# Kernel tuning notes

Hardware: AMD Instinct MI355X
Metric: run time of the kernel (lower is better)

Reference implementation:

```python
import jax, jax.numpy as jnp
import numpy as np
import math

B, T, O = 4, 1024, 128
D, H, L, V = 512, 8, 6, 128
M, EH = 100000, 4
EHD = D // EH
HD = D // H
TK = O + 2 * T
PAD_ID = 0
NGRAM = 4

def _primes():
    ps = []
    base = 131
    for h in range(EH):
        x = base + h * 1009
        row = []
        for _ in range(NGRAM):
            row.append(x % (2 ** 32))
            x = x * 31 + 1
        ps.append(row)
    return jnp.array(ps, dtype=jnp.uint32)

PRIMES = _primes()

def rmsnorm(x, scale, eps=1e-6):
    return x / jnp.sqrt(jnp.mean(jnp.square(x), axis=-1, keepdims=True) + eps) * scale

def precompute_freqs_cis(dim, max_len, theta=10000.0):
    freqs = 1.0 / theta ** (jnp.arange(0, dim, 2, dtype=jnp.float32) / dim)
    t = jnp.arange(max_len, dtype=jnp.float32)
    return jnp.exp(1j * jnp.outer(t, freqs))[None, :, None, :]  # (1, max_len, 1, dim/2)

def apply_rope(x, f):
    b, t, h, d = x.shape
    xc = jax.lax.complex(x[..., 0::2], x[..., 1::2])
    xr = xc * f
    return jnp.stack([xr.real, xr.imag], axis=-1).reshape(b, t, h, d)

def setup_inputs() -> dict:
    key = jax.random.key(0)
    ks = jax.random.split(key, 16)
    rn = lambda k, shp, s=0.02: jax.random.normal(k, shp, jnp.float32) * s
    logit = lambda p: float(np.log(p / (1.0 - p)))
    return {
        'tokens_w': jax.random.randint(ks[0], (B, T), 0, V, dtype=jnp.int32),
        'mem_ids': jax.random.randint(ks[1], (B, O), 0, V, dtype=jnp.int32),
        'mem_emb': jax.random.normal(ks[2], (B, O, D), jnp.float32),
        'ssum': jax.random.normal(ks[3], (B, D), jnp.float32),
        'embed_table': rn(ks[4], (V, D)),
        'engram_table': rn(ks[5], (M, EH, EHD)),
        'engram_gate': jnp.full((EH, EHD), -2.0, jnp.float32),
        'engram_scale': jnp.ones(D, jnp.float32),
        'mem_W': rn(ks[6], (D, D)), 'mem_b': jnp.zeros(D, jnp.float32),
        'mem_scale': jnp.ones(D, jnp.float32),
        'alpha_gate': jnp.full((D,), logit(0.1), jnp.float32),
        'ssum_W': rn(ks[7], (D, D)),
        'ln1': jnp.ones((L, D), jnp.float32),
        'qW': rn(ks[8], (L, D, D)), 'qb': jnp.zeros((L, D), jnp.float32),
        'kW': rn(ks[9], (L, D, D)), 'kb': jnp.zeros((L, D), jnp.float32),
        'vW': rn(ks[10], (L, D, D)), 'vb': jnp.zeros((L, D), jnp.float32),
        'oW': rn(ks[11], (L, D, D)), 'ob': jnp.zeros((L, D), jnp.float32),
        'ln2': jnp.ones((L, D), jnp.float32),
        'w_in': rn(ks[12], (L, D, 8 * D)),
        'w_out': rn(ks[13], (L, 4 * D, D)),
        'final_scale': jnp.ones(D, jnp.float32),
    }

def _forward(tokens_w, mem_ids, mem_emb, ssum, embed_table, engram_table, engram_gate,
             engram_scale, mem_W, mem_b, mem_scale, alpha_gate, ssum_W,
             ln1, qW, qb, kW, kb, vW, vb, oW, ob, ln2, w_in, w_out, final_scale):
    # token embedding
    x = embed_table[tokens_w]  # (B,T,D)
    # multi-head engram: rolling n-gram hash lookup
    cur = jnp.where(tokens_w == PAD_ID, 0, tokens_w).astype(jnp.uint32)
    prev = jnp.where(mem_ids == PAD_ID, 0, mem_ids).astype(jnp.uint32)
    full = jnp.concatenate([prev, cur], axis=1)  # (B, O+T)
    hs = jnp.zeros((B, T, EH), jnp.uint32)
    for i in range(NGRAM):
        chunk = full[:, O - i: O + T - i]
        hs = hs + chunk[:, :, None] * PRIMES[None, None, :, i]
    idx = (hs % jnp.uint32(M)).astype(jnp.int32)  # (B,T,EH)
    retr = engram_table[idx, jnp.arange(EH)[None, None, :], :]  # (B,T,EH,EHD)
    eng = (retr * jax.nn.sigmoid(engram_gate)[None, None]).reshape(B, T, D)
    eng = rmsnorm(eng, engram_scale)
    # memory adapter + state-sum injection
    mem_p = rmsnorm(mem_emb @ mem_W + mem_b, mem_scale)
    alpha = jax.nn.sigmoid(alpha_gate)
    x = x + (ssum @ ssum_W)[:, None, :] * alpha[None, None, :]
    kv_seq = jnp.concatenate([mem_p, eng, x], axis=1)  # (B, TK, D)
    # masks: mem fully visible, engram + current causal; pad invalid keys
    tril = jnp.tril(jnp.ones((T, T), bool))
    full_mask = jnp.concatenate([jnp.ones((T, O), bool), tril, tril], axis=1)
    valid_curr = tokens_w != PAD_ID
    valid_k = jnp.concatenate([jnp.ones((B, O), bool), valid_curr, valid_curr], axis=1)
    mask = full_mask[None, None] & valid_k[:, None, None, :]  # (B,1,T,TK)
    freqs = precompute_freqs_cis(HD, TK + 32)
    fq, fk = freqs[:, :T], freqs[:, :TK]
    scale = 1.0 / math.sqrt(HD)

    def block(cx, p):
        ln1_, qW_, qb_, kW_, kb_, vW_, vb_, oW_, ob_, ln2_, wi_, wo_ = p
        nx = rmsnorm(cx, ln1_)
        q = (nx @ qW_ + qb_).reshape(B, T, H, HD)
        k = (kv_seq @ kW_ + kb_).reshape(B, TK, H, HD)
        v = (kv_seq @ vW_ + vb_).reshape(B, TK, H, HD)
        q = apply_rope(q, fq)
        k = apply_rope(k, fk)
        scores = jnp.einsum('bqhd,bkhd->bhqk', q, k) * scale
        scores = jnp.where(mask, scores, -1e9)
        probs = jax.nn.softmax(scores, axis=-1)
        o = jnp.einsum('bhqk,bkhd->bqhd', probs, v).reshape(B, T, D)
        cx = cx + o @ oW_ + ob_
        n2 = rmsnorm(cx, ln2_)
        gate, val = jnp.split(n2 @ wi_, 2, axis=-1)
        cx = cx + (jax.nn.silu(gate) * val) @ wo_
        return cx, None

    curr_x, _ = jax.lax.scan(block, x, (ln1, qW, qb, kW, kb, vW, vb, oW, ob, ln2, w_in, w_out))
    return rmsnorm(curr_x, final_scale)

def reference(tokens_w, mem_ids, mem_emb, ssum, embed_table, engram_table, engram_gate,
              engram_scale, mem_W, mem_b, mem_scale, alpha_gate, ssum_W,
              ln1, qW, qb, kW, kb, vW, vb, oW, ob, ln2, w_in, w_out, final_scale):
    return _forward(tokens_w, mem_ids, mem_emb, ssum, embed_table, engram_table, engram_gate,
                    engram_scale, mem_W, mem_b, mem_scale, alpha_gate, ssum_W,
                    ln1, qW, qb, kW, kb, vW, vb, oW, ob, ln2, w_in, w_out, final_scale)
```

## Files before the change

### kernel.cpp

```cpp
#include <hip/hip_runtime.h>
#include <hip/hip_bf16.h>
#include <math.h>

#define B_ 4
#define T_ 1024
#define O_ 128
#define D_ 512
#define H_ 8
#define L_ 6
#define TK_ 2176
#define MM_ 100000
#define EH_ 4
#define EHD_ 128
#define HD_ 64

typedef float f32x4 __attribute__((ext_vector_type(4)));
typedef short bf16x8 __attribute__((ext_vector_type(8)));
typedef unsigned short u16;

__device__ __constant__ unsigned int PRIMES_[4][4] = {
  {131u,  4062u,  125923u, 3903614u},
  {1140u, 35341u, 1095572u, 33962733u},
  {2149u, 66620u, 2065221u, 64021852u},
  {3158u, 97899u, 3034870u, 94080971u},
};

__device__ __forceinline__ float wave_sum_f(float v) {
  #pragma unroll
  for (int off = 32; off; off >>= 1) v += __shfl_xor(v, off);
  return v;
}

__device__ __forceinline__ short f2bf(float f) {
  unsigned int u = __float_as_uint(f);
  unsigned int r = (u + 0x7fffu + ((u >> 16) & 1u)) >> 16;
  return (short)r;
}

__device__ __forceinline__ void gload16(const void* g, void* l) {
  __builtin_amdgcn_global_load_lds((const __attribute__((address_space(1))) void*)g,
                                   (__attribute__((address_space(3))) void*)l, 16, 0, 0);
}

__global__ __launch_bounds__(64) void rope_table_k(float* __restrict__ rc,
                                                   float* __restrict__ rs) {
  int i = blockIdx.x * 64 + threadIdx.x;
  int t = i >> 5, j = i & 31;
  float freq = __powf(10000.0f, -(float)j / 32.0f);
  float ang = (float)t * freq;
  rc[i] = cosf(ang);
  rs[i] = sinf(ang);
}

__global__ __launch_bounds__(256) void ssum_proj_k(const float* __restrict__ ssum,
                                                   const float* __restrict__ sW,
                                                   float* __restrict__ ssp) {
  int col = blockIdx.x * 256 + threadIdx.x;
  int b = blockIdx.y;
  float acc = 0.f;
  for (int d = 0; d < D_; ++d) acc += ssum[b * D_ + d] * sW[(size_t)d * D_ + col];
  ssp[b * D_ + col] = acc;
}

__global__ __launch_bounds__(256) void sgemm_k(const float* __restrict__ A,
                                               const float* __restrict__ W,
                                               const float* __restrict__ bias,
                                               float* __restrict__ C,
                                               int M, int N, int K) {
  __shared__ float As[16][68];
  __shared__ float Bs[16][68];
  int tid = threadIdx.x;
  int row0 = blockIdx.y * 64;
  int col0 = blockIdx.x * 64;
  int tx = tid & 15, ty = tid >> 4;
  int am = tid >> 2, ak = (tid & 3) * 4;
  int bk = tid >> 4, bc = (tid & 15) * 4;
  float acc[4][4] = {};
  for (int k0 = 0; k0 < K; k0 += 16) {
    float4 av = *reinterpret_cast<const float4*>(&A[(size_t)(row0 + am) * K + k0 + ak]);
    As[ak + 0][am] = av.x; As[ak + 1][am] = av.y; As[ak + 2][am] = av.z; As[ak + 3][am] = av.w;
    float4 bv = *reinterpret_cast<const float4*>(&W[(size_t)(k0 + bk) * N + col0 + bc]);
    *reinterpret_cast<float4*>(&Bs[bk][bc]) = bv;
    __syncthreads();
    #pragma unroll
    for (int kk = 0; kk < 16; ++kk) {
      float4 a4 = *reinterpret_cast<const float4*>(&As[kk][ty * 4]);
      float4 b4 = *reinterpret_cast<const float4*>(&Bs[kk][tx * 4]);
      float a[4] = {a4.x, a4.y, a4.z, a4.w};
      float b[4] = {b4.x, b4.y, b4.z, b4.w};
      #pragma unroll
      for (int i = 0; i < 4; ++i)
        #pragma unroll
        for (int j = 0; j < 4; ++j) acc[i][j] += a[i] * b[j];
    }
    __syncthreads();
  }
  int cbase = col0 + tx * 4;
  float4 b4 = *reinterpret_cast<const float4*>(&bias[cbase]);
  float bb[4] = {b4.x, b4.y, b4.z, b4.w};
  #pragma unroll
  for (int i = 0; i < 4; ++i) {
    int row = row0 + ty * 4 + i;
    *reinterpret_cast<float4*>(&C[(size_t)row * N + cbase]) =
        make_float4(acc[i][0] + bb[0], acc[i][1] + bb[1], acc[i][2] + bb[2], acc[i][3] + bb[3]);
  }
}

__device__ __forceinline__ void wconv_tile(const float* __restrict__ W, u16* __restrict__ wT,
                                           int K, int N) {
  __shared__ float s[64][65];
  int n0 = blockIdx.x * 64, k0 = blockIdx.y * 64;
  int tid = threadIdx.x;
  int kr = tid >> 4, nc = (tid & 15) * 4;
  #pragma unroll
  for (int kk = 0; kk < 4; ++kk) {
    float4 f = *reinterpret_cast<const float4*>(&W[(size_t)(k0 + kr + kk * 16) * N + n0 + nc]);
    s[kr + kk * 16][nc + 0] = f.x; s[kr + kk * 16][nc + 1] = f.y;
    s[kr + kk * 16][nc + 2] = f.z; s[kr + kk * 16][nc + 3] = f.w;
  }
  __syncthreads();
  int nr = tid >> 4, kc = (tid & 15) * 4;
  #pragma unroll
  for (int nn = 0; nn < 4; ++nn) {
    int n = nr + nn * 16;
    ushort4 o;
    o.x = (u16)f2bf(s[kc + 0][n]); o.y = (u16)f2bf(s[kc + 1][n]);
    o.z = (u16)f2bf(s[kc + 2][n]); o.w = (u16)f2bf(s[kc + 3][n]);
    *reinterpret_cast<ushort4*>(&wT[(size_t)(n0 + n) * K + k0 + kc]) = o;
  }
}

__global__ __launch_bounds__(256) void wconv_qkvo_k(const float* __restrict__ qW,
                                                    const float* __restrict__ kW,
                                                    const float* __restrict__ vW,
                                                    const float* __restrict__ oW,
                                                    u16* __restrict__ dst) {
  int z = blockIdx.z;
  int l = z >> 2, which = z & 3;
  const float* src = which == 0 ? qW : which == 1 ? kW : which == 2 ? vW : oW;
  wconv_tile(src + (size_t)l * D_ * D_, dst + (size_t)z * D_ * D_, D_, D_);
}

__global__ __launch_bounds__(256) void wconv_win_k(const float* __restrict__ w_in,
                                                   u16* __restrict__ dst) {
  int l = blockIdx.z;
  wconv_tile(w_in + (size_t)l * 512 * 4096, dst + (size_t)l * 4096 * 512, 512, 4096);
}

__global__ __launch_bounds__(256) void wconv_wout_k(const float* __restrict__ w_out,
                                                    u16* __restrict__ dst) {
  int l = blockIdx.z;
  wconv_tile(w_out + (size_t)l * 2048 * 512, dst + (size_t)l * 512 * 2048, 2048, 512);
}

template<int EPI>
__global__ __launch_bounds__(256) void gemm_sm_k(const u16* __restrict__ A,
                                                 const u16* __restrict__ Bt,
                                                 const float* __restrict__ bias,
                                                 void* __restrict__ Cout,
                                                 int M, int N, int K, int posmod,
                                                 const float* __restrict__ rc,
                                                 const float* __restrict__ rs) {
  __shared__ __align__(16) u16 As[2][64 * 32];
  __shared__ __align__(16) u16 Bs[2][64 * 32];
  int tid = threadIdx.x;
  int w = tid >> 6, lane = tid & 63;
  int lr = lane & 15, lg = lane >> 4;
  int row0 = blockIdx.y * 64, col0 = blockIdx.x * 64;
  int wr = w >> 1, wc = w & 1;
  f32x4 acc[2][2] = {};

  int srow = tid >> 2;
  int skel = (tid & 3) * 8;

  auto stage = [&](int buf, int k0) {
    gload16(A + (size_t)(row0 + srow) * K + k0 + skel, &As[buf][srow * 32 + skel]);
    gload16(Bt + (size_t)(col0 + srow) * K + k0 + skel, &Bs[buf][srow * 32 + skel]);
  };

  stage(0, 0);
  __syncthreads();
  int nk = K >> 5;
  int buf = 0;
  for (int t = 0; t < nk; ++t) {
    if (t + 1 < nk) stage(buf ^ 1, (t + 1) * 32);
    bf16x8 af[2], bf[2];
    #pragma unroll
    for (int i = 0; i < 2; ++i)
      af[i] = *reinterpret_cast<const bf16x8*>(&As[buf][(wr * 32 + i * 16 + lr) * 32 + lg * 8]);
    #pragma unroll
    for (int j = 0; j < 2; ++j)
      bf[j] = *reinterpret_cast<const bf16x8*>(&Bs[buf][(wc * 32 + j * 16 + lr) * 32 + lg * 8]);
    #pragma unroll
    for (int i = 0; i < 2; ++i)
      #pragma unroll
      for (int j = 0; j < 2; ++j)
        acc[i][j] = __builtin_amdgcn_mfma_f32_16x16x32_bf16(af[i], bf[j], acc[i][j], 0, 0, 0);
    __syncthreads();
    buf ^= 1;
  }

  #pragma unroll
  for (int j = 0; j < 2; ++j) {
    int col = col0 + wc * 32 + j * 16 + lr;
    float bs = bias ? bias[col] : 0.f;
    #pragma unroll
    for (int i = 0; i < 2; ++i) {
      #pragma unroll
      for (int r = 0; r < 4; ++r) {
        int row = row0 + wr * 32 + i * 16 + lg * 4 + r;
        float v = acc[i][j][r] + bs;
        if (EPI == 1) {
          int pos = row % posmod;
          int d = col & 63;
          float c = rc[(size_t)pos * 32 + (d >> 1)];
          float s = rs[(size_t)pos * 32 + (d >> 1)];
          float partner = __shfl_xor(v, 1);
          v = (d & 1) ? (partner * s + v * c) : (v * c - partner * s);
        }
        if (EPI == 2) {
          float* Cf = (float*)Cout;
          Cf[(size_t)row * N + col] += v;
        } else {
          u16* Cb = (u16*)Cout;
          Cb[(size_t)row * N + col] = (u16)f2bf(v);
        }
      }
    }
  }
}

__global__ __launch_bounds__(256) void kv_gemm_k(const u16* __restrict__ A,
                                                 const u16* __restrict__ wqkvoT,
                                                 const float* __restrict__ kbias_all,
                                                 const float* __restrict__ vbias_all,
                                                 u16* __restrict__ kb_base,
                                                 u16* __restrict__ vb_base,
                                                 const float* __restrict__ rc,
                                                 const float* __restrict__ rs,
                                                 int l0, size_t ostride) {
  __shared__ __align__(16) u16 As[2][128 * 32];
  __shared__ __align__(16) u16 Bk[2][64 * 32];
  __shared__ __align__(16) u16 Bv[2][64 * 32];
  const int K = 512, N = 512;
  int l = l0 + blockIdx.z;
  const u16* wkT = wqkvoT + ((size_t)l * 4 + 1) * (D_ * D_);
  const u16* wvT = wqkvoT + ((size_t)l * 4 + 2) * (D_ * D_);
  const float* kbias = kbias_all + l * D_;
  const float* vbias = vbias_all + l * D_;
  u16* kb = kb_base + (size_t)blockIdx.z * ostride;
  u16* vb = vb_base + (size_t)blockIdx.z * ostride;
  int tid = threadIdx.x;
  int w = tid >> 6, lane = tid & 63;
  int lr = lane & 15, lg = lane >> 4;
  int row0 = blockIdx.y * 128, col0 = blockIdx.x * 64;
  int wr = w >> 1, wc = w & 1;
  f32x4 ak_[4][2] = {};
  f32x4 av_[4][2] = {};

  int srow = lane >> 2;
  int skel = (lane & 3) * 8;

  auto stage = [&](int buf, int k0) {
    #pragma unroll
    for (int ci = 0; ci < 2; ++ci) {
      int c = w * 2 + ci;
      gload16(A + (size_t)(row0 + c * 16 + srow) * K + k0 + skel, &As[buf][c * 512]);
    }
    gload16(wkT + (size_t)(col0 + w * 16 + srow) * K + k0 + skel, &Bk[buf][w * 512]);
    gload16(wvT + (size_t)(col0 + w * 16 + srow) * K + k0 + skel, &Bv[buf][w * 512]);
  };

  stage(0, 0);
  __syncthreads();
  int buf = 0;
  for (int t = 0; t < 16; ++t) {
    if (t + 1 < 16) stage(buf ^ 1, (t + 1) * 32);
    bf16x8 af[4], bk[2], bv[2];
    #pragma unroll
    for (int i = 0; i < 4; ++i)
      af[i] = *reinterpret_cast<const bf16x8*>(&As[buf][(wr * 64 + i * 16 + lr) * 32 + lg * 8]);
    #pragma unroll
    for (int j = 0; j < 2; ++j) {
      bk[j] = *reinterpret_cast<const bf16x8*>(&Bk[buf][(wc * 32 + j * 16 + lr) * 32 + lg * 8]);
      bv[j] = *reinterpret_cast<const bf16x8*>(&Bv[buf][(wc * 32 + j * 16 + lr) * 32 + lg * 8]);
    }
    #pragma unroll
    for (int i = 0; i < 4; ++i)
      #pragma unroll
      for (int j = 0; j < 2; ++j) {
        ak_[i][j] = __builtin_amdgcn_mfma_f32_16x16x32_bf16(af[i], bk[j], ak_[i][j], 0, 0, 0);
        av_[i][j] = __builtin_amdgcn_mfma_f32_16x16x32_bf16(af[i], bv[j], av_[i][j], 0, 0, 0);
      }
    __syncthreads();
    buf ^= 1;
  }

  u16* stg = &As[0][0];
  __syncthreads();
  #pragma unroll
  for (int pass = 0; pass < 2; ++pass) {
    #pragma unroll
    for (int j = 0; j < 2; ++j) {
      int lcol = wc * 32 + j * 16 + lr;
      int gcol = col0 + lcol;
      float bs = pass ? vbias[gcol] : kbias[gcol];
      int d = gcol & 63;
      #pragma unroll
      for (int i = 0; i < 4; ++i) {
        #pragma unroll
        for (int r = 0; r < 4; ++r) {
          int lrow = wr * 64 + i * 16 + lg * 4 + r;
          float v = (pass ? av_[i][j][r] : ak_[i][j][r]) + bs;
          if (!pass) {
            int pos = (row0 + lrow) % TK_;
            float c = rc[(size_t)pos * 32 + (d >> 1)];
            float s = rs[(size_t)pos * 32 + (d >> 1)];
            float partner = __shfl_xor(v, 1);
            v = (d & 1) ? (partner * s + v * c) : (v * c - partner * s);
          }
          stg[lrow * 64 + lcol] = (u16)f2bf(v);
        }
      }
    }
    __syncthreads();
    {
      int trow = tid >> 1, tc0 = (tid & 1) * 32;
      u16* dst = (pass ? vb : kb) + (size_t)(row0 + trow) * N + col0 + tc0;
      const u16* src = &stg[trow * 64 + tc0];
      #pragma unroll
      for (int c = 0; c < 4; ++c)
        *reinterpret_cast<bf16x8*>(dst + c * 8) = *reinterpret_cast<const bf16x8*>(src + c * 8);
    }
    __syncthreads();
  }
}

__global__ __launch_bounds__(256) void mlp_in_mfma_k(const u16* __restrict__ A,
                                                     const u16* __restrict__ wiT,
                                                     u16* __restrict__ Hout) {
  __shared__ __align__(16) u16 As[2][128 * 32];
  __shared__ __align__(16) u16 Bg[2][64 * 32];
  __shared__ __align__(16) u16 Bv[2][64 * 32];
  int tid = threadIdx.x;
  int w = tid >> 6, lane = tid & 63;
  int lr = lane & 15, lg = lane >> 4;
  int hc0 = blockIdx.x * 64, row0 = blockIdx.y * 128;
  int wr = w >> 1, wc = w & 1;
  f32x4 ag[4][2] = {};
  f32x4 av[4][2] = {};
  const int K = 512;

  int srow = lane >> 2;
  int skel = (lane & 3) * 8;

  auto stage = [&](int buf, int k0) {
    #pragma unroll
    for (int ci = 0; ci < 2; ++ci) {
      int c = w * 2 + ci;
      gload16(A + (size_t)(row0 + c * 16 + srow) * K + k0 + skel, &As[buf][c * 512]);
    }
    gload16(wiT + (size_t)(hc0 + w * 16 + srow) * K + k0 + skel, &Bg[buf][w * 512]);
    gload16(wiT + (size_t)(2048 + hc0 + w * 16 + srow) * K + k0 + skel, &Bv[buf][w * 512]);
  };

  stage(0, 0);
  __syncthreads();
  int buf = 0;
  for (int t = 0; t < 16; ++t) {
    if (t + 1 < 16) stage(buf ^ 1, (t + 1) * 32);
    bf16x8 af[4], bg[2], bv[2];
    #pragma unroll
    for (int i = 0; i < 4; ++i)
      af[i] = *reinterpret_cast<const bf16x8*>(&As[buf][(wr * 64 + i * 16 + lr) * 32 + lg * 8]);
    #pragma unroll
    for (int j = 0; j < 2; ++j) {
      bg[j] = *reinterpret_cast<const bf16x8*>(&Bg[buf][(wc * 32 + j * 16 + lr) * 32 + lg * 8]);
      bv[j] = *reinterpret_cast<const bf16x8*>(&Bv[buf][(wc * 32 + j * 16 + lr) * 32 + lg * 8]);
    }
    #pragma unroll
    for (int i = 0; i < 4; ++i)
      #pragma unroll
      for (int j = 0; j < 2; ++j) {
        ag[i][j] = __builtin_amdgcn_mfma_f32_16x16x32_bf16(af[i], bg[j], ag[i][j], 0, 0, 0);
        av[i][j] = __builtin_amdgcn_mfma_f32_16x16x32_bf16(af[i], bv[j], av[i][j], 0, 0, 0);
      }
    __syncthreads();
    buf ^= 1;
  }

  #pragma unroll
  for (int j = 0; j < 2; ++j) {
    int col = hc0 + wc * 32 + j * 16 + lr;
    #pragma unroll
    for (int i = 0; i < 4; ++i) {
      #pragma unroll
      for (int r = 0; r < 4; ++r) {
        int row = row0 + wr * 64 + i * 16 + lg * 4 + r;
        float g = ag[i][j][r];
        float sg = g / (1.f + __expf(-g));
        Hout[(size_t)row * 2048 + col] = (u16)f2bf(sg * av[i][j][r]);
      }
    }
  }
}

template<int OUTBF>
__global__ __launch_bounds__(128) void rmsnorm_k(const float* __restrict__ in,
                                                 const float* __restrict__ scale,
                                                 void* __restrict__ out) {
  int row = blockIdx.x;
  int tid = threadIdx.x;
  float4 v = *reinterpret_cast<const float4*>(&in[(size_t)row * D_ + tid * 4]);
  float ss = v.x * v.x + v.y * v.y + v.z * v.z + v.w * v.w;
  ss = wave_sum_f(ss);
  __shared__ float red[2];
  if ((tid & 63) == 0) red[tid >> 6] = ss;
  __syncthreads();
  ss = red[0] + red[1];
  float inv = 1.0f / sqrtf(ss / (float)D_ + 1e-6f);
  float4 sc = *reinterpret_cast<const float4*>(&scale[tid * 4]);
  float o0 = v.x * inv * sc.x, o1 = v.y * inv * sc.y, o2 = v.z * inv * sc.z, o3 = v.w * inv * sc.w;
  if (OUTBF) {
    ushort4 o;
    o.x = (u16)f2bf(o0); o.y = (u16)f2bf(o1); o.z = (u16)f2bf(o2); o.w = (u16)f2bf(o3);
    *reinterpret_cast<ushort4*>((u16*)out + (size_t)row * D_ + tid * 4) = o;
  } else {
    *reinterpret_cast<float4*>((float*)out + (size_t)row * D_ + tid * 4) =
        make_float4(o0, o1, o2, o3);
  }
}

__global__ __launch_bounds__(128) void memnorm_k(const float* __restrict__ tmp,
                                                 const float* __restrict__ scale,
                                                 u16* __restrict__ kv) {
  int o = blockIdx.x, b = blockIdx.y;
  int tid = threadIdx.x;
  float4 v = *reinterpret_cast<const float4*>(&tmp[(size_t)(b * O_ + o) * D_ + tid * 4]);
  float ss = v.x * v.x + v.y * v.y + v.z * v.z + v.w * v.w;
  ss = wave_sum_f(ss);
  __shared__ float red[2];
  if ((tid & 63) == 0) red[tid >> 6] = ss;
  __syncthreads();
  ss = red[0] + red[1];
  float inv = 1.0f / sqrtf(ss / (float)D_ + 1e-6f);
  float4 sc = *reinterpret_cast<const float4*>(&scale[tid * 4]);
  ushort4 oo;
  oo.x = (u16)f2bf(v.x * inv * sc.x); oo.y = (u16)f2bf(v.y * inv * sc.y);
  oo.z = (u16)f2bf(v.z * inv * sc.z); oo.w = (u16)f2bf(v.w * inv * sc.w);
  *reinterpret_cast<ushort4*>(&kv[(size_t)(b * TK_ + o) * D_ + tid * 4]) = oo;
}

__global__ __launch_bounds__(128) void engram_k(const int* __restrict__ tokens,
                                                const int* __restrict__ mem_ids,
                                                const float* __restrict__ etab,
                                                const float* __restrict__ egate,
                                                const float* __restrict__ escale,
                                                u16* __restrict__ kv) {
  int t = blockIdx.x, b = blockIdx.y;
  int tid = threadIdx.x;
  unsigned int toks[4];
  #pragma unroll
  for (int i = 0; i < 4; ++i) {
    int idx = t - i;
    toks[i] = (idx >= 0) ? (unsigned int)tokens[b * T_ + idx]
                         : (unsigned int)mem_ids[b * O_ + O_ + idx];
  }
  int c = tid * 4;
  int h = c >> 7;
  int e = c & 127;
  unsigned int hs = 0;
  #pragma unroll
  for (int i = 0; i < 4; ++i) hs += toks[i] * PRIMES_[h][i];
  int idxh = (int)(hs % (unsigned int)MM_);
  float4 r = *reinterpret_cast<const float4*>(&etab[((size_t)idxh * EH_ + h) * EHD_ + e]);
  float4 g = *reinterpret_cast<const float4*>(&egate[h * EHD_ + e]);
  float4 val;
  val.x = r.x / (1.f + __expf(-g.x));
  val.y = r.y / (1.f + __expf(-g.y));
  val.z = r.z / (1.f + __expf(-g.z));
  val.w = r.w / (1.f + __expf(-g.w));
  float ss = val.x * val.x + val.y * val.y + val.z * val.z + val.w * val.w;
  ss = wave_sum_f(ss);
  __shared__ float red[2];
  if ((tid & 63) == 0) red[tid >> 6] = ss;
  __syncthreads();
  ss = red[0] + red[1];
  float inv = 1.0f / sqrtf(ss / (float)D_ + 1e-6f);
  float4 sc = *reinterpret_cast<const float4*>(&escale[c]);
  ushort4 oo;
  oo.x = (u16)f2bf(val.x * inv * sc.x); oo.y = (u16)f2bf(val.y * inv * sc.y);
  oo.z = (u16)f2bf(val.z * inv * sc.z); oo.w = (u16)f2bf(val.w * inv * sc.w);
  *reinterpret_cast<ushort4*>(&kv[(size_t)(b * TK_ + O_ + t) * D_ + c]) = oo;
}

__global__ __launch_bounds__(128) void embed_k(const int* __restrict__ tokens,
                                               const float* __restrict__ etab,
                                               const float* __restrict__ ssp,
                                               const float* __restrict__ alpha_g,
                                               float* __restrict__ cx,
                                               u16* __restrict__ kv) {
  int t = blockIdx.x, b = blockIdx.y;
  int tid = threadIdx.x;
  int c = tid * 4;
  int tok = tokens[b * T_ + t];
  float4 e = *reinterpret_cast<const float4*>(&etab[(size_t)tok * D_ + c]);
  float4 sp = *reinterpret_cast<const float4*>(&ssp[b * D_ + c]);
  float4 ag = *reinterpret_cast<const float4*>(&alpha_g[c]);
  float4 x;
  x.x = e.x + sp.x / (1.f + __expf(-ag.x));
  x.y = e.y + sp.y / (1.f + __expf(-ag.y));
  x.z = e.z + sp.z / (1.f + __expf(-ag.z));
  x.w = e.w + sp.w / (1.f + __expf(-ag.w));
  *reinterpret_cast<float4*>(&cx[(size_t)(b * T_ + t) * D_ + c]) = x;
  ushort4 oo;
  oo.x = (u16)f2bf(x.x); oo.y = (u16)f2bf(x.y);
  oo.z = (u16)f2bf(x.z); oo.w = (u16)f2bf(x.w);
  *reinterpret_cast<ushort4*>(&kv[(size_t)(b * TK_ + O_ + T_ + t) * D_ + c]) = oo;
}

#define KIDX8(r, c) (((r) << 6) + ((c) ^ (((r) & 7) << 3)))
#define KIDX4(r, c) (((r) << 6) + ((c) ^ (((r) & 15) << 2)))
#define PIDX(q, o) (((q) << 5) + ((o) ^ (((q) & 7) << 2)))

__global__ __launch_bounds__(512) void attn_mfma_k(const u16* __restrict__ qb,
                                                   const u16* __restrict__ kb,
                                                   const u16* __restrict__ vb,
                                                   const int* __restrict__ tokens,
                                                   u16* __restrict__ ob) {
  __shared__ __align__(16) short ks[2][64 * 64];
  __shared__ __align__(16) short vst[2][64 * 64];
  __shared__ __align__(16) unsigned int pbuf[8][16 * 32];
  __shared__ unsigned char vtok[T_];

  int fid = blockIdx.x;
  int h = fid & 7;
  int s = fid >> 3;
  int pair = s & 7;
  int b = s >> 3;
  int bxA = pair, bxB = 15 - pair;

  int tid = threadIdx.x;
  int w = tid >> 6, lane = tid & 63;
  int lr = lane & 15;
  int lg = lane >> 4;
  int myBx = (w < 4) ? bxA : bxB;
  int qw0 = myBx * 64 + (w & 3) * 16;
  int tq = qw0 + lr;

  for (int i = tid; i < T_; i += 512) vtok[i] = (tokens[b * T_ + i] != 0);

  bf16x8 aq[2];
  {
    const u16* qp = &qb[((size_t)(b * T_) + tq) * D_ + h * 64];
    aq[0] = *reinterpret_cast<const bf16x8*>(qp + lg * 8);
    aq[1] = *reinterpret_cast<const bf16x8*>(qp + 32 + lg * 8);
  }

  float m_ = -1e30f, lsum = 0.f;
  f32x4 od[4];
  #pragma unroll
  for (int dt = 0; dt < 4; ++dt) od[dt] = (f32x4){0.f, 0.f, 0.f, 0.f};

  int sr = tid >> 3;
  int sc = (tid & 7) * 8;
  int vr2 = (tid >> 4) * 2;
  int vc = (tid & 15) * 4;

  int nt = 2 + 2 * (bxB + 1);
  auto tile_pos = [&](int i, int& pos0, int& base, bool& masked, bool& part) {
    if (i < 2) { pos0 = i * 64; base = 0; masked = false; part = true; }
    else if (i < 3 + bxB) {
      int t = i - 2;
      pos0 = O_ + t * 64; base = O_; masked = true; part = (t <= myBx);
    } else {
      int t = i - (3 + bxB);
      pos0 = O_ + T_ + t * 64; base = O_ + T_; masked = true; part = (t <= myBx);
    }
  };

  bf16x8 pk0;
  short4 pv0, pv1;

  auto load_regs = [&](int pos0) {
    const u16* kg = &kb[((size_t)(b * TK_) + pos0 + sr) * D_ + h * 64 + sc];
    pk0 = *reinterpret_cast<const bf16x8*>(kg);
    const u16* vg = &vb[((size_t)(b * TK_) + pos0 + vr2) * D_ + h * 64 + vc];
    pv0 = *reinterpret_cast<const short4*>(vg);
    pv1 = *reinterpret_cast<const short4*>(vg + D_);
  };

  auto write_lds = [&](int buf) {
    *reinterpret_cast<bf16x8*>(&ks[buf][KIDX8(sr, sc)]) = pk0;
    unsigned int t0 = (unsigned int)(u16)pv0.x | ((unsigned int)(u16)pv1.x << 16);
    unsigned int t1 = (unsigned int)(u16)pv0.y | ((unsigned int)(u16)pv1.y << 16);
    unsigned int t2 = (unsigned int)(u16)pv0.z | ((unsigned int)(u16)pv1.z << 16);
    unsigned int t3 = (unsigned int)(u16)pv0.w | ((unsigned int)(u16)pv1.w << 16);
    *reinterpret_cast<unsigned int*>(&vst[buf][KIDX4(vc + 0, vr2)]) = t0;
    *reinterpret_cast<unsigned int*>(&vst[buf][KIDX4(vc + 1, vr2)]) = t1;
    *reinterpret_cast<unsigned int*>(&vst[buf][KIDX4(vc + 2, vr2)]) = t2;
    *reinterpret_cast<unsigned int*>(&vst[buf][KIDX4(vc + 3, vr2)]) = t3;
  };

  unsigned int* pw = (unsigned int*)pbuf[w];

  auto compute = [&](int buf, int pos0, int base, bool masked) {
    float sv[4][4];
    __builtin_amdgcn_s_setprio(1);
    #pragma unroll
    for (int kt = 0; kt < 4; ++kt) {
      bf16x8 ka0 = *reinterpret_cast<const bf16x8*>(&ks[buf][KIDX8(kt * 16 + lr, lg * 8)]);
      bf16x8 ka1 = *reinterpret_cast<const bf16x8*>(&ks[buf][KIDX8(kt * 16 + lr, 32 + lg * 8)]);
      f32x4 sf = (f32x4){0.f, 0.f, 0.f, 0.f};
      sf = __builtin_amdgcn_mfma_f32_16x16x32_bf16(ka0, aq[0], sf, 0, 0, 0);
      sf = __builtin_amdgcn_mfma_f32_16x16x32_bf16(ka1, aq[1], sf, 0, 0, 0);
      #pragma unroll
      for (int r = 0; r < 4; ++r) sv[kt][r] = sf[r];
    }
    __builtin_amdgcn_s_setprio(0);
    if (masked) {
      #pragma unroll
      for (int kt = 0; kt < 4; ++kt) {
        #pragma unroll
        for (int r = 0; r < 4; ++r) {
          int tk = pos0 + kt * 16 + lg * 4 + r - base;
          bool valid = (vtok[tk] != 0) && (tk <= tq);
          sv[kt][r] = valid ? sv[kt][r] * 0.125f : -1e30f;
        }
      }
    } else {
      #pragma unroll
      for (int kt = 0; kt < 4; ++kt)
        #pragma unroll
        for (int r = 0; r < 4; ++r) sv[kt][r] *= 0.125f;
    }
    float pmax = sv[0][0];
    #pragma unroll
    for (int kt = 0; kt < 4; ++kt)
      #pragma unroll
      for (int r = 0; r < 4; ++r) pmax = fmaxf(pmax, sv[kt][r]);
    pmax = fmaxf(pmax, __shfl_xor(pmax, 16));
    pmax = fmaxf(pmax, __shfl_xor(pmax, 32));
    float mnew = fmaxf(m_, pmax);
    float al = __expf(m_ - mnew);
    m_ = mnew;
    float psum = 0.f;
    #pragma unroll
    for (int kt = 0; kt < 4; ++kt)
      #pragma unroll
      for (int r = 0; r < 4; ++r) {
        float pe = __expf(sv[kt][r] - mnew);
        sv[kt][r] = pe;
        psum += pe;
      }
    psum += __shfl_xor(psum, 16);
    psum += __shfl_xor(psum, 32);
    lsum = lsum * al + psum;
    #pragma unroll
    for (int dt = 0; dt < 4; ++dt) {
      f32x4 o = od[dt];
      o[0] *= al; o[1] *= al; o[2] *= al; o[3] *= al;
      od[dt] = o;
    }
    #pragma unroll
    for (int kt = 0; kt < 4; ++kt) {
      uint2 wp;
      asm("v_cvt_pk_bf16_f32 %0, %1, %2" : "=v"(wp.x) : "v"(sv[kt][0]), "v"(sv[kt][1]));
      asm("v_cvt_pk_bf16_f32 %0, %1, %2" : "=v"(wp.y) : "v"(sv[kt][2]), "v"(sv[kt][3]));
      *reinterpret_cast<uint2*>(&pw[PIDX(lr, kt * 8 + lg * 2)]) = wp;
    }
    bf16x8 pf0 = *reinterpret_cast<const bf16x8*>(&pw[PIDX(lr, lg * 4)]);
    bf16x8 pf1 = *reinterpret_cast<const bf16x8*>(&pw[PIDX(lr, 16 + lg * 4)]);
    __builtin_amdgcn_s_setprio(1);
    #pragma unroll
    for (int dt = 0; dt < 4; ++dt) {
      short4 lo0 = *reinterpret_cast<const short4*>(&vst[buf][KIDX4(dt * 16 + lr, lg * 8)]);
      short4 hi0 = *reinterpret_cast<const short4*>(&vst[buf][KIDX4(dt * 16 + lr, lg * 8 + 4)]);
      short4 lo1 = *reinterpret_cast<const short4*>(&vst[buf][KIDX4(dt * 16 + lr, 32 + lg * 8)]);
      short4 hi1 = *reinterpret_cast<const short4*>(&vst[buf][KIDX4(dt * 16 + lr, 36 + lg * 8)]);
      bf16x8 va0 = {lo0.x, lo0.y, lo0.z, lo0.w, hi0.x, hi0.y, hi0.z, hi0.w};
      bf16x8 va1 = {lo1.x, lo1.y, lo1.z, lo1.w, hi1.x, hi1.y, hi1.z, hi1.w};
      od[dt] = __builtin_amdgcn_mfma_f32_16x16x32_bf16(va0, pf0, od[dt], 0, 0, 0);
      od[dt] = __builtin_amdgcn_mfma_f32_16x16x32_bf16(va1, pf1, od[dt], 0, 0, 0);
    }
    __builtin_amdgcn_s_setprio(0);
  };

  {
    int pos0, base; bool masked, part;
    tile_pos(0, pos0, base, masked, part);
    load_regs(pos0);
  }
  for (int i = 0; i < nt; ++i) {
    write_lds(i & 1);
    __syncthreads();
    int pos0, base; bool masked, part;
    tile_pos(i, pos0, base, masked, part);
    if (i + 1 < nt) {
      int npos, nbase; bool nmask, npart;
      tile_pos(i + 1, npos, nbase, nmask, npart);
      load_regs(npos);
    }
    if (part) compute(i & 1, pos0, base, masked);
  }

  float inv = 1.0f / lsum;
  #pragma unroll
  for (int dt = 0; dt < 4; ++dt) {
    ushort4 o4;
    o4.x = (u16)f2bf(od[dt][0] * inv);
    o4.y = (u16)f2bf(od[dt][1] * inv);
    o4.z = (u16)f2bf(od[dt][2] * inv);
    o4.w = (u16)f2bf(od[dt][3] * inv);
    *reinterpret_cast<ushort4*>(
        &ob[((size_t)(b * T_) + tq) * D_ + h * 64 + dt * 16 + lg * 4]) = o4;
  }
}

extern "C" void kernel_launch(void* const* d_in, const int* in_sizes, int n_in,
                              void* d_out, int out_size, void* d_ws, size_t ws_size,
                              hipStream_t stream) {
  (void)in_sizes; (void)n_in; (void)out_size;
  const int* tokens = (const int*)d_in[0];
  const int* mem_ids = (const int*)d_in[1];
  const float* mem_emb = (const float*)d_in[2];
  const float* ssum = (const float*)d_in[3];
  const float* embed = (const float*)d_in[4];
  const float* engram_t = (const float*)d_in[5];
  const float* engram_g = (const float*)d_in[6];
  const float* engram_s = (const float*)d_in[7];
  const float* mem_W = (const float*)d_in[8];
  const float* mem_b = (const float*)d_in[9];
  const float* mem_s = (const float*)d_in[10];
  const float* alpha_g = (const float*)d_in[11];
  const float* ssum_W = (const float*)d_in[12];
  const float* ln1 = (const float*)d_in[13];
  const float* qW = (const float*)d_in[14];
  const float* qbias = (const float*)d_in[15];
  const float* kW = (const float*)d_in[16];
  const float* kbias = (const float*)d_in[17];
  const float* vW = (const float*)d_in[18];
  const float* vbias = (const float*)d_in[19];
  const float* oW = (const float*)d_in[20];
  const float* obias = (const float*)d_in[21];
  const float* ln2 = (const float*)d_in[22];
  const float* w_in = (const float*)d_in[23];
  const float* w_out = (const float*)d_in[24];
  const float* final_s = (const float*)d_in[25];

  const size_t KVSZ = (size_t)B_ * TK_ * D_;
  size_t need = (KVSZ * 2 * 2 * L_) + 120u * 1024 * 1024;
  bool batched = ws_size >= need;

  char* p = (char*)d_ws;
  auto alloc = [&](size_t bytes) { char* r = p; p += (bytes + 255) & ~(size_t)255; return r; };
  u16* kv_b   = (u16*)alloc(KVSZ * 2);
  float* cx   = (float*)alloc((size_t)B_ * T_ * D_ * 4);
  u16* nx_b   = (u16*)alloc((size_t)B_ * T_ * D_ * 2);
  u16* qb_b   = (u16*)alloc((size_t)B_ * T_ * D_ * 2);
  int nkv = batched ? L_ : 1;
  u16* kb_all = (u16*)alloc(KVSZ * 2 * nkv);
  u16* vb_all = (u16*)alloc(KVSZ * 2 * nkv);
  u16* hb;
  if (batched) hb = (u16*)alloc((size_t)B_ * T_ * 2048 * 2);
  else hb = kb_all;
  u16* wqkvoT = (u16*)alloc((size_t)L_ * 4 * D_ * D_ * 2);
  u16* wiT    = (u16*)alloc((size_t)L_ * 4096 * 512 * 2);
  u16* woutT  = (u16*)alloc((size_t)L_ * 512 * 2048 * 2);
  float* ssp  = (float*)alloc((size_t)B_ * D_ * 4);
  float* rc   = (float*)alloc((size_t)TK_ * 32 * 4);
  float* rs   = (float*)alloc((size_t)TK_ * 32 * 4);
  float* mem_tmp = (float*)qb_b;
  u16* ob_b = nx_b;

  rope_table_k<<<TK_ * 32 / 64, 64, 0, stream>>>(rc, rs);
  wconv_qkvo_k<<<dim3(8, 8, L_ * 4), 256, 0, stream>>>(qW, kW, vW, oW, wqkvoT);
  wconv_win_k<<<dim3(64, 8, L_), 256, 0, stream>>>(w_in, wiT);
  wconv_wout_k<<<dim3(8, 32, L_), 256, 0, stream>>>(w_out, woutT);
  ssum_proj_k<<<dim3(2, B_), 256, 0, stream>>>(ssum, ssum_W, ssp);
  sgemm_k<<<dim3(8, 8), 256, 0, stream>>>(mem_emb, mem_W, mem_b, mem_tmp, B_ * O_, D_, D_);
  memnorm_k<<<dim3(O_, B_), 128, 0, stream>>>(mem_tmp, mem_s, kv_b);
  engram_k<<<dim3(T_, B_), 128, 0, stream>>>(tokens, mem_ids, engram_t, engram_g, engram_s, kv_b);
  embed_k<<<dim3(T_, B_), 128, 0, stream>>>(tokens, embed, ssp, alpha_g, cx, kv_b);

  if (batched) {
    kv_gemm_k<<<dim3(8, 68, L_), 256, 0, stream>>>(kv_b, wqkvoT, kbias, vbias,
                                                   kb_all, vb_all, rc, rs, 0, KVSZ);
  }

  const size_t WSZ = (size_t)D_ * D_;
  for (int l = 0; l < L_; ++l) {
    const u16* wqT = wqkvoT + ((size_t)l * 4 + 0) * WSZ;
    const u16* woT = wqkvoT + ((size_t)l * 4 + 3) * WSZ;
    const u16* wil = wiT + (size_t)l * 4096 * 512;
    const u16* wol = woutT + (size_t)l * 512 * 2048;
    u16* kb_l = batched ? kb_all + (size_t)l * KVSZ : kb_all;
    u16* vb_l = batched ? vb_all + (size_t)l * KVSZ : vb_all;

    rmsnorm_k<1><<<B_ * T_, 128, 0, stream>>>(cx, ln1 + l * D_, nx_b);
    gemm_sm_k<1><<<dim3(8, 64), 256, 0, stream>>>(nx_b, wqT, qbias + l * D_, qb_b,
                                                  B_ * T_, D_, D_, T_, rc, rs);
    if (!batched) {
      kv_gemm_k<<<dim3(8, 68, 1), 256, 0, stream>>>(kv_b, wqkvoT, kbias, vbias,
                                                    kb_l, vb_l, rc, rs, l, 0);
    }
    attn_mfma_k<<<dim3(256), 512, 0, stream>>>(qb_b, kb_l, vb_l, tokens, ob_b);
    gemm_sm_k<2><<<dim3(8, 64), 256, 0, stream>>>(ob_b, woT, obias + l * D_, cx,
                                                  B_ * T_, D_, D_, 0, nullptr, nullptr);
    rmsnorm_k<1><<<B_ * T_, 128, 0, stream>>>(cx, ln2 + l * D_, nx_b);
    mlp_in_mfma_k<<<dim3(32, 32), 256, 0, stream>>>(nx_b, wil, hb);
    gemm_sm_k<2><<<dim3(8, 64), 256, 0, stream>>>(hb, wol, nullptr, cx,
                                                  B_ * T_, D_, 2048, 0, nullptr, nullptr);
  }
  rmsnorm_k<0><<<B_ * T_, 128, 0, stream>>>(cx, final_s, d_out);
}
```

Before: 1.088 ms.

## Remap KV GEMM grid for locality, store epilogue directly, prefetch two attention tiles

The KV projection kernel moves to a 1-D grid and remaps block indices so that groups of 8 row-tiles sharing a column tile run together, with out-of-range blocks exiting early. Its epilogue drops the LDS staging and the extra barriers, writing K (with RoPE applied) and V straight to global memory as scattered 2-byte stores. The attention kernel now keeps two register sets of prefetched K/V and unrolls the loop by two, so global loads are issued two tiles ahead. The aim is better L2 reuse and more latency hiding, at the cost of uncoalesced stores and higher register pressure.

```diff
diff --git a/kernel.cpp b/kernel.cpp
--- a/kernel.cpp
+++ b/kernel.cpp
@@ -243,17 +243,25 @@
   __shared__ __align__(16) u16 Bk[2][64 * 32];
   __shared__ __align__(16) u16 Bv[2][64 * 32];
   const int K = 512, N = 512;
-  int l = l0 + blockIdx.z;
+  int bid = blockIdx.x;
+  int c_ = bid & 7;
+  int x_ = (bid >> 3) & 7;
+  int rest = bid >> 6;
+  int yh = rest % 9;
+  int z = rest / 9;
+  int y_ = yh * 8 + c_;
+  if (y_ >= 68) return;
+  int l = l0 + z;
   const u16* wkT = wqkvoT + ((size_t)l * 4 + 1) * (D_ * D_);
   const u16* wvT = wqkvoT + ((size_t)l * 4 + 2) * (D_ * D_);
   const float* kbias = kbias_all + l * D_;
   const float* vbias = vbias_all + l * D_;
-  u16* kb = kb_base + (size_t)blockIdx.z * ostride;
-  u16* vb = vb_base + (size_t)blockIdx.z * ostride;
+  u16* kb = kb_base + (size_t)z * ostride;
+  u16* vb = vb_base + (size_t)z * ostride;
   int tid = threadIdx.x;
   int w = tid >> 6, lane = tid & 63;
   int lr = lane & 15, lg = lane >> 4;
-  int row0 = blockIdx.y * 128, col0 = blockIdx.x * 64;
+  int row0 = y_ * 128, col0 = x_ * 64;
   int wr = w >> 1, wc = w & 1;
   f32x4 ak_[4][2] = {};
   f32x4 av_[4][2] = {};
@@ -296,43 +304,26 @@
     buf ^= 1;
   }
 
-  u16* stg = &As[0][0];
-  __syncthreads();
-  #pragma unroll
-  for (int pass = 0; pass < 2; ++pass) {
-    #pragma unroll
-    for (int j = 0; j < 2; ++j) {
-      int lcol = wc * 32 + j * 16 + lr;
-      int gcol = col0 + lcol;
-      float bs = pass ? vbias[gcol] : kbias[gcol];
-      int d = gcol & 63;
-      #pragma unroll
-      for (int i = 0; i < 4; ++i) {
-        #pragma unroll
-        for (int r = 0; r < 4; ++r) {
-          int lrow = wr * 64 + i * 16 + lg * 4 + r;
-          float v = (pass ? av_[i][j][r] : ak_[i][j][r]) + bs;
-          if (!pass) {
-            int pos = (row0 + lrow) % TK_;
-            float c = rc[(size_t)pos * 32 + (d >> 1)];
-            float s = rs[(size_t)pos * 32 + (d >> 1)];
-            float partner = __shfl_xor(v, 1);
-            v = (d & 1) ? (partner * s + v * c) : (v * c - partner * s);
-          }
-          stg[lrow * 64 + lcol] = (u16)f2bf(v);
-        }
+  #pragma unroll
+  for (int j = 0; j < 2; ++j) {
+    int col = col0 + wc * 32 + j * 16 + lr;
+    float kbs = kbias[col], vbs = vbias[col];
+    int d = col & 63;
+    #pragma unroll
+    for (int i = 0; i < 4; ++i) {
+      #pragma unroll
+      for (int r = 0; r < 4; ++r) {
+        int row = row0 + wr * 64 + i * 16 + lg * 4 + r;
+        int pos = row % TK_;
+        float vk = ak_[i][j][r] + kbs;
+        float c = rc[(size_t)pos * 32 + (d >> 1)];
+        float s = rs[(size_t)pos * 32 + (d >> 1)];
+        float partner = __shfl_xor(vk, 1);
+        vk = (d & 1) ? (partner * s + vk * c) : (vk * c - partner * s);
+        kb[(size_t)row * N + col] = (u16)f2bf(vk);
+        vb[(size_t)row * N + col] = (u16)f2bf(av_[i][j][r] + vbs);
       }
     }
-    __syncthreads();
-    {
-      int trow = tid >> 1, tc0 = (tid & 1) * 32;
-      u16* dst = (pass ? vb : kb) + (size_t)(row0 + trow) * N + col0 + tc0;
-      const u16* src = &stg[trow * 64 + tc0];
-      #pragma unroll
-      for (int c = 0; c < 4; ++c)
-        *reinterpret_cast<bf16x8*>(dst + c * 8) = *reinterpret_cast<const bf16x8*>(src + c * 8);
-    }
-    __syncthreads();
   }
 }
 
@@ -579,19 +570,19 @@
     }
   };
 
-  bf16x8 pk0;
-  short4 pv0, pv1;
-
-  auto load_regs = [&](int pos0) {
+  bf16x8 pkA, pkB;
+  short4 pv0A, pv1A, pv0B, pv1B;
+
+  auto load_regs = [&](int pos0, bf16x8& pk, short4& v0, short4& v1) {
     const u16* kg = &kb[((size_t)(b * TK_) + pos0 + sr) * D_ + h * 64 + sc];
-    pk0 = *reinterpret_cast<const bf16x8*>(kg);
+    pk = *reinterpret_cast<const bf16x8*>(kg);
     const u16* vg = &vb[((size_t)(b * TK_) + pos0 + vr2) * D_ + h * 64 + vc];
-    pv0 = *reinterpret_cast<const short4*>(vg);
-    pv1 = *reinterpret_cast<const short4*>(vg + D_);
+    v0 = *reinterpret_cast<const short4*>(vg);
+    v1 = *reinterpret_cast<const short4*>(vg + D_);
   };
 
-  auto write_lds = [&](int buf) {
-    *reinterpret_cast<bf16x8*>(&ks[buf][KIDX8(sr, sc)]) = pk0;
+  auto write_lds = [&](int buf, bf16x8 pk, short4 pv0, short4 pv1) {
+    *reinterpret_cast<bf16x8*>(&ks[buf][KIDX8(sr, sc)]) = pk;
     unsigned int t0 = (unsigned int)(u16)pv0.x | ((unsigned int)(u16)pv1.x << 16);
     unsigned int t1 = (unsigned int)(u16)pv0.y | ((unsigned int)(u16)pv1.y << 16);
     unsigned int t2 = (unsigned int)(u16)pv0.z | ((unsigned int)(u16)pv1.z << 16);
@@ -689,19 +680,35 @@
   {
     int pos0, base; bool masked, part;
     tile_pos(0, pos0, base, masked, part);
-    load_regs(pos0);
-  }
-  for (int i = 0; i < nt; ++i) {
-    write_lds(i & 1);
+    load_regs(pos0, pkA, pv0A, pv1A);
+    tile_pos(1, pos0, base, masked, part);
+    load_regs(pos0, pkB, pv0B, pv1B);
+  }
+  for (int i = 0; i < nt; i += 2) {
+    write_lds(0, pkA, pv0A, pv1A);
     __syncthreads();
-    int pos0, base; bool masked, part;
-    tile_pos(i, pos0, base, masked, part);
-    if (i + 1 < nt) {
-      int npos, nbase; bool nmask, npart;
-      tile_pos(i + 1, npos, nbase, nmask, npart);
-      load_regs(npos);
-    }
-    if (part) compute(i & 1, pos0, base, masked);
+    {
+      int pos0, base; bool masked, part;
+      tile_pos(i, pos0, base, masked, part);
+      if (i + 2 < nt) {
+        int npos, nb; bool nm, np;
+        tile_pos(i + 2, npos, nb, nm, np);
+        load_regs(npos, pkA, pv0A, pv1A);
+      }
+      if (part) compute(0, pos0, base, masked);
+    }
+    write_lds(1, pkB, pv0B, pv1B);
+    __syncthreads();
+    {
+      int pos0, base; bool masked, part;
+      tile_pos(i + 1, pos0, base, masked, part);
+      if (i + 3 < nt) {
+        int npos, nb; bool nm, np;
+        tile_pos(i + 3, npos, nb, nm, np);
+        load_regs(npos, pkB, pv0B, pv1B);
+      }
+      if (part) compute(1, pos0, base, masked);
+    }
   }
 
   float inv = 1.0f / lsum;
@@ -784,8 +791,8 @@
   embed_k<<<dim3(T_, B_), 128, 0, stream>>>(tokens, embed, ssp, alpha_g, cx, kv_b);
 
   if (batched) {
-    kv_gemm_k<<<dim3(8, 68, L_), 256, 0, stream>>>(kv_b, wqkvoT, kbias, vbias,
-                                                   kb_all, vb_all, rc, rs, 0, KVSZ);
+    kv_gemm_k<<<dim3(8 * 8 * 9 * L_), 256, 0, stream>>>(kv_b, wqkvoT, kbias, vbias,
+                                                        kb_all, vb_all, rc, rs, 0, KVSZ);
   }
 
   const size_t WSZ = (size_t)D_ * D_;
@@ -801,8 +808,8 @@
     gemm_sm_k<1><<<dim3(8, 64), 256, 0, stream>>>(nx_b, wqT, qbias + l * D_, qb_b,
                                                   B_ * T_, D_, D_, T_, rc, rs);
     if (!batched) {
-      kv_gemm_k<<<dim3(8, 68, 1), 256, 0, stream>>>(kv_b, wqkvoT, kbias, vbias,
-                                                    kb_l, vb_l, rc, rs, l, 0);
+      kv_gemm_k<<<dim3(8 * 8 * 9), 256, 0, stream>>>(kv_b, wqkvoT, kbias, vbias,
+                                                     kb_l, vb_l, rc, rs, l, 0);
     }
     attn_mfma_k<<<dim3(256), 512, 0, stream>>>(qb_b, kb_l, vb_l, tokens, ob_b);
     gemm_sm_k<2><<<dim3(8, 64), 256, 0, stream>>>(ob_b, woT, obias + l * D_, cx,
```

After: 1.052 ms. 1.03x faster.
